# Optimization experiments

Hardware: AMD Instinct MI355X
Metric: run time of the kernel (lower is better)

## Reference

```python
import jax, jax.numpy as jnp
import numpy as np

N_NODES = 100000
N_EDGES = 600000
D_FEAT = 128
OUT_DIM = 128


def setup_inputs() -> dict:
    key = jax.random.key(0)
    k_x, k_r, k_c, k_v, k_w = jax.random.split(key, 5)
    x = jax.random.normal(k_x, (N_NODES, D_FEAT), dtype=jnp.float32)
    adj_rows = jax.random.randint(k_r, (N_EDGES,), 0, N_NODES, dtype=jnp.int64 if jax.config.jax_enable_x64 else jnp.int32).astype(jnp.int32)
    adj_cols = jax.random.randint(k_c, (N_EDGES,), 0, N_NODES, dtype=jnp.int32)
    adj_vals = jax.random.uniform(k_v, (N_EDGES,), dtype=jnp.float32)
    # Xavier-uniform init for W of shape [2*d, out]
    fan_in, fan_out = 2 * D_FEAT, OUT_DIM
    bound = float(np.sqrt(6.0 / (fan_in + fan_out)))
    W = jax.random.uniform(k_w, (2 * D_FEAT, OUT_DIM), minval=-bound, maxval=bound, dtype=jnp.float32)
    return {"x": x, "adj_rows": adj_rows, "adj_cols": adj_cols, "adj_vals": adj_vals, "W": W}


def reference(x, adj_rows, adj_cols, adj_vals, W):
    # h = A @ x  via COO SpMM: gather neighbor features, scale, segment-sum by row
    msgs = adj_vals[:, None] * x[adj_cols]            # [E, d]
    h = jax.ops.segment_sum(msgs, adj_rows, num_segments=N_NODES)  # [N, d]
    # concat([h, x]) @ W == h @ W[:d] + x @ W[d:]  (avoids materializing concat)
    out = h @ W[:D_FEAT] + x @ W[D_FEAT:]             # [N, out]
    return jax.nn.relu(out)
```

## Files before the change

### kernel.cpp

```cpp
#include <hip/hip_runtime.h>
#include <hip/hip_bf16.h>

constexpr int N_NODES = 100000;
constexpr int N_EDGES = 600000;
constexpr int D = 128;
constexpr int CAP = 32;

constexpr size_t X16_OFF  = 0;
constexpr size_t WP_OFF   = 25600000;
constexpr size_t CNT_OFF  = 25665536;
constexpr size_t BINS_OFF = 26065536;

typedef __attribute__((ext_vector_type(8))) short short8;
typedef __attribute__((ext_vector_type(4))) float float4v;

__device__ inline unsigned short f2bf(float f) {
    union { float f; unsigned int u; } v; v.f = f;
    unsigned int u = v.u + 0x7fffu + ((v.u >> 16) & 1u);
    return (unsigned short)(u >> 16);
}
__device__ inline float bf2f(unsigned int lo16) {
    union { unsigned int u; float f; } v; v.u = lo16 << 16;
    return v.f;
}

__global__ __launch_bounds__(256) void prep_kernel(
    const float* __restrict__ x, uint4* __restrict__ x16,
    const float* __restrict__ W, unsigned short* __restrict__ Wp,
    const int* __restrict__ rows, const int* __restrict__ cols,
    const float* __restrict__ vals,
    int* __restrict__ cnt, int2* __restrict__ bins)
{
    const int tid = blockIdx.x * 256 + threadIdx.x;
    const int T   = gridDim.x * 256;

    for (int e = tid; e < N_EDGES; e += T) {
        int r = rows[e];
        int pos = atomicAdd(&cnt[r], 1);
        if (pos < CAP)
            bins[(size_t)r * CAP + pos] = make_int2(cols[e], __float_as_int(vals[e]));
    }

    for (int idx = tid; idx < 8 * 8 * 64 * 8; idx += T) {
        int j    = idx & 7;
        int lane = (idx >> 3) & 63;
        int jt   = (idx >> 9) & 7;
        int s    = idx >> 12;
        int k = s * 32 + (lane >> 4) * 8 + j;
        int n = jt * 16 + (lane & 15);
        Wp[idx] = f2bf(W[k * 128 + n]);
    }

    for (int g = tid; g < N_NODES * D / 8; g += T) {
        const float4* xp = reinterpret_cast<const float4*>(x + (size_t)g * 8);
        float4 a = xp[0], c = xp[1];
        uint4 o;
        o.x = (unsigned int)f2bf(a.x) | ((unsigned int)f2bf(a.y) << 16);
        o.y = (unsigned int)f2bf(a.z) | ((unsigned int)f2bf(a.w) << 16);
        o.z = (unsigned int)f2bf(c.x) | ((unsigned int)f2bf(c.y) << 16);
        o.w = (unsigned int)f2bf(c.z) | ((unsigned int)f2bf(c.w) << 16);
        x16[g] = o;
    }
}

__global__ __launch_bounds__(128) void fused_agg_gemm_kernel(
    const uint4* __restrict__ x16v,
    const unsigned short* __restrict__ x16s,
    const int* __restrict__ cnt,
    const int2* __restrict__ bins,
    const unsigned short* __restrict__ Wp,
    float* __restrict__ out)
{
    __shared__ uint4 lds4[2 * 256];

    const int tid  = threadIdx.x;
    const int wave = tid >> 6;
    const int lane = tid & 63;
    const int row0 = blockIdx.x * 32 + wave * 16;

    {
        const int g   = lane >> 4;
        const int gl  = lane & 15;
        const int s_w = gl >> 2;
        const int q_w = gl & 3;

        int dends[4];
        const int4* b2[4];
        #pragma unroll
        for (int t = 0; t < 4; t++) {
            const int n = row0 + t * 4 + g;
            int d = cnt[n];
            dends[t] = d > CAP ? CAP : d;
            b2[t] = reinterpret_cast<const int4*>(bins + (size_t)n * CAP);
        }

        int4 nb0 = b2[0][0], nb1 = b2[0][1], nb2 = b2[0][2], nb3 = b2[0][3];

        #pragma unroll
        for (int t = 0; t < 4; t++) {
            const int m_local = t * 4 + g;
            const int dend = dends[t];

            const int4 c0 = nb0, c1 = nb1, c2 = nb2, c3 = nb3;
            if (t < 3) {
                nb0 = b2[t + 1][0]; nb1 = b2[t + 1][1];
                nb2 = b2[t + 1][2]; nb3 = b2[t + 1][3];
            }

            int col0 = c0.x; col0 = col0 < 0 ? 0 : col0;
            col0 = col0 >= N_NODES ? N_NODES - 1 : col0;
            const int cc1 = (1 < dend) ? c0.z : col0;
            const int cc2 = (2 < dend) ? c1.x : col0;
            const int cc3 = (3 < dend) ? c1.z : col0;
            const int cc4 = (4 < dend) ? c2.x : col0;
            const int cc5 = (5 < dend) ? c2.z : col0;
            const int cc6 = (6 < dend) ? c3.x : col0;
            const int cc7 = (7 < dend) ? c3.z : col0;
            const float v0 = (0 < dend) ? __int_as_float(c0.y) : 0.f;
            const float v1 = (1 < dend) ? __int_as_float(c0.w) : 0.f;
            const float v2 = (2 < dend) ? __int_as_float(c1.y) : 0.f;
            const float v3 = (3 < dend) ? __int_as_float(c1.w) : 0.f;
            const float v4 = (4 < dend) ? __int_as_float(c2.y) : 0.f;
            const float v5 = (5 < dend) ? __int_as_float(c2.w) : 0.f;
            const float v6 = (6 < dend) ? __int_as_float(c3.y) : 0.f;
            const float v7 = (7 < dend) ? __int_as_float(c3.w) : 0.f;

            const uint4 p0 = x16v[(size_t)col0 * 16 + gl];
            const uint4 p1 = x16v[(size_t)cc1  * 16 + gl];
            const uint4 p2 = x16v[(size_t)cc2  * 16 + gl];
            const uint4 p3 = x16v[(size_t)cc3  * 16 + gl];
            const uint4 p4 = x16v[(size_t)cc4  * 16 + gl];
            const uint4 p5 = x16v[(size_t)cc5  * 16 + gl];
            const uint4 p6 = x16v[(size_t)cc6  * 16 + gl];
            const uint4 p7 = x16v[(size_t)cc7  * 16 + gl];

            float a0, a1, a2, a3, a4, a5, a6, a7;
            a0  = v0 * bf2f(p0.x & 0xffffu) + v1 * bf2f(p1.x & 0xffffu)
                + v2 * bf2f(p2.x & 0xffffu) + v3 * bf2f(p3.x & 0xffffu)
                + v4 * bf2f(p4.x & 0xffffu) + v5 * bf2f(p5.x & 0xffffu)
                + v6 * bf2f(p6.x & 0xffffu) + v7 * bf2f(p7.x & 0xffffu);
            a1  = v0 * bf2f(p0.x >> 16)     + v1 * bf2f(p1.x >> 16)
                + v2 * bf2f(p2.x >> 16)     + v3 * bf2f(p3.x >> 16)
                + v4 * bf2f(p4.x >> 16)     + v5 * bf2f(p5.x >> 16)
                + v6 * bf2f(p6.x >> 16)     + v7 * bf2f(p7.x >> 16);
            a2  = v0 * bf2f(p0.y & 0xffffu) + v1 * bf2f(p1.y & 0xffffu)
                + v2 * bf2f(p2.y & 0xffffu) + v3 * bf2f(p3.y & 0xffffu)
                + v4 * bf2f(p4.y & 0xffffu) + v5 * bf2f(p5.y & 0xffffu)
                + v6 * bf2f(p6.y & 0xffffu) + v7 * bf2f(p7.y & 0xffffu);
            a3  = v0 * bf2f(p0.y >> 16)     + v1 * bf2f(p1.y >> 16)
                + v2 * bf2f(p2.y >> 16)     + v3 * bf2f(p3.y >> 16)
                + v4 * bf2f(p4.y >> 16)     + v5 * bf2f(p5.y >> 16)
                + v6 * bf2f(p6.y >> 16)     + v7 * bf2f(p7.y >> 16);
            a4  = v0 * bf2f(p0.z & 0xffffu) + v1 * bf2f(p1.z & 0xffffu)
                + v2 * bf2f(p2.z & 0xffffu) + v3 * bf2f(p3.z & 0xffffu)
                + v4 * bf2f(p4.z & 0xffffu) + v5 * bf2f(p5.z & 0xffffu)
                + v6 * bf2f(p6.z & 0xffffu) + v7 * bf2f(p7.z & 0xffffu);
            a5  = v0 * bf2f(p0.z >> 16)     + v1 * bf2f(p1.z >> 16)
                + v2 * bf2f(p2.z >> 16)     + v3 * bf2f(p3.z >> 16)
                + v4 * bf2f(p4.z >> 16)     + v5 * bf2f(p5.z >> 16)
                + v6 * bf2f(p6.z >> 16)     + v7 * bf2f(p7.z >> 16);
            a6  = v0 * bf2f(p0.w & 0xffffu) + v1 * bf2f(p1.w & 0xffffu)
                + v2 * bf2f(p2.w & 0xffffu) + v3 * bf2f(p3.w & 0xffffu)
                + v4 * bf2f(p4.w & 0xffffu) + v5 * bf2f(p5.w & 0xffffu)
                + v6 * bf2f(p6.w & 0xffffu) + v7 * bf2f(p7.w & 0xffffu);
            a7  = v0 * bf2f(p0.w >> 16)     + v1 * bf2f(p1.w >> 16)
                + v2 * bf2f(p2.w >> 16)     + v3 * bf2f(p3.w >> 16)
                + v4 * bf2f(p4.w >> 16)     + v5 * bf2f(p5.w >> 16)
                + v6 * bf2f(p6.w >> 16)     + v7 * bf2f(p7.w >> 16);

            if (dend > 8) {
                const int2* bp = bins + (size_t)(row0 + m_local) * CAP;
                for (int i = 8; i < dend; i += 4) {
                    const int i1 = (i + 1 < dend) ? i + 1 : dend - 1;
                    const int i2 = (i + 2 < dend) ? i + 2 : dend - 1;
                    const int i3 = (i + 3 < dend) ? i + 3 : dend - 1;
                    int2 e0 = bp[i];
                    int2 e1 = bp[i1];
                    int2 e2 = bp[i2];
                    int2 e3 = bp[i3];
                    uint4 q0 = x16v[(size_t)e0.x * 16 + gl];
                    uint4 q1 = x16v[(size_t)e1.x * 16 + gl];
                    uint4 q2 = x16v[(size_t)e2.x * 16 + gl];
                    uint4 q3 = x16v[(size_t)e3.x * 16 + gl];
                    float w0 = __int_as_float(e0.y);
                    float w1 = (i + 1 < dend) ? __int_as_float(e1.y) : 0.f;
                    float w2 = (i + 2 < dend) ? __int_as_float(e2.y) : 0.f;
                    float w3 = (i + 3 < dend) ? __int_as_float(e3.y) : 0.f;
                    a0 += w0 * bf2f(q0.x & 0xffffu) + w1 * bf2f(q1.x & 0xffffu)
                        + w2 * bf2f(q2.x & 0xffffu) + w3 * bf2f(q3.x & 0xffffu);
                    a1 += w0 * bf2f(q0.x >> 16)     + w1 * bf2f(q1.x >> 16)
                        + w2 * bf2f(q2.x >> 16)     + w3 * bf2f(q3.x >> 16);
                    a2 += w0 * bf2f(q0.y & 0xffffu) + w1 * bf2f(q1.y & 0xffffu)
                        + w2 * bf2f(q2.y & 0xffffu) + w3 * bf2f(q3.y & 0xffffu);
                    a3 += w0 * bf2f(q0.y >> 16)     + w1 * bf2f(q1.y >> 16)
                        + w2 * bf2f(q2.y >> 16)     + w3 * bf2f(q3.y >> 16);
                    a4 += w0 * bf2f(q0.z & 0xffffu) + w1 * bf2f(q1.z & 0xffffu)
                        + w2 * bf2f(q2.z & 0xffffu) + w3 * bf2f(q3.z & 0xffffu);
                    a5 += w0 * bf2f(q0.z >> 16)     + w1 * bf2f(q1.z >> 16)
                        + w2 * bf2f(q2.z >> 16)     + w3 * bf2f(q3.z >> 16);
                    a6 += w0 * bf2f(q0.w & 0xffffu) + w1 * bf2f(q1.w & 0xffffu)
                        + w2 * bf2f(q2.w & 0xffffu) + w3 * bf2f(q3.w & 0xffffu);
                    a7 += w0 * bf2f(q0.w >> 16)     + w1 * bf2f(q1.w >> 16)
                        + w2 * bf2f(q2.w >> 16)     + w3 * bf2f(q3.w >> 16);
                }
            }

            uint4 o;
            o.x = (unsigned int)f2bf(a0) | ((unsigned int)f2bf(a1) << 16);
            o.y = (unsigned int)f2bf(a2) | ((unsigned int)f2bf(a3) << 16);
            o.z = (unsigned int)f2bf(a4) | ((unsigned int)f2bf(a5) << 16);
            o.w = (unsigned int)f2bf(a6) | ((unsigned int)f2bf(a7) << 16);
            lds4[wave * 256 + s_w * 64 + m_local * 4 + q_w] = o;
        }
    }
    __syncthreads();

    const int m    = lane & 15;
    const int quad = lane >> 4;

    const unsigned short* xrow = x16s + (size_t)(row0 + m) * D + quad * 8;

    float4v acc[8];
    #pragma unroll
    for (int jt = 0; jt < 8; jt++) acc[jt] = (float4v){0.f, 0.f, 0.f, 0.f};

    #pragma unroll
    for (int s = 0; s < 8; s++) {
        short8 a;
        if (s < 4)
            a = *reinterpret_cast<const short8*>(&lds4[wave * 256 + s * 64 + m * 4 + quad]);
        else
            a = *reinterpret_cast<const short8*>(xrow + (s - 4) * 32);
        #pragma unroll
        for (int jt = 0; jt < 8; jt++) {
            short8 b = *reinterpret_cast<const short8*>(
                Wp + ((size_t)((s * 8 + jt) * 64 + lane)) * 8);
            acc[jt] = __builtin_amdgcn_mfma_f32_16x16x32_bf16(a, b, acc[jt], 0, 0, 0);
        }
    }

    #pragma unroll
    for (int reg = 0; reg < 4; reg++) {
        const int r = row0 + quad * 4 + reg;
        float* orow = out + (size_t)r * D;
        #pragma unroll
        for (int jt = 0; jt < 8; jt++)
            orow[jt * 16 + m] = fmaxf(acc[jt][reg], 0.f);
    }
}

extern "C" void kernel_launch(void* const* d_in, const int* in_sizes, int n_in,
                              void* d_out, int out_size, void* d_ws, size_t ws_size,
                              hipStream_t stream)
{
    const float* x    = (const float*)d_in[0];
    const int*   rows = (const int*)  d_in[1];
    const int*   cols = (const int*)  d_in[2];
    const float* vals = (const float*)d_in[3];
    const float* W    = (const float*)d_in[4];
    float* out = (float*)d_out;

    char* ws = (char*)d_ws;
    uint4*          x16v = (uint4*)         (ws + X16_OFF);
    unsigned short* x16s = (unsigned short*)(ws + X16_OFF);
    unsigned short* Wp   = (unsigned short*)(ws + WP_OFF);
    int*            cnt  = (int*)           (ws + CNT_OFF);
    int2*           bins = (int2*)          (ws + BINS_OFF);

    hipMemsetAsync(cnt, 0, N_NODES * sizeof(int), stream);
    prep_kernel<<<2048, 256, 0, stream>>>(x, x16v, W, Wp, rows, cols, vals, cnt, bins);
    fused_agg_gemm_kernel<<<N_NODES / 32, 128, 0, stream>>>(
        x16v, x16s, cnt, bins, Wp, out);
}
```

Measured before the change: 185.2 us.

## Partition edge binning by row range and split GEMM columns across waves

```diff
diff --git a/kernel.cpp b/kernel.cpp
--- a/kernel.cpp
+++ b/kernel.cpp
@@ -5,6 +5,8 @@
 constexpr int N_EDGES = 600000;
 constexpr int D = 128;
 constexpr int CAP = 32;
+constexpr int NRANGE = 8;
+constexpr int ROWS_PER_RANGE = N_NODES / NRANGE;
 
 constexpr size_t X16_OFF  = 0;
 constexpr size_t WP_OFF   = 25600000;
@@ -34,13 +36,6 @@
     const int tid = blockIdx.x * 256 + threadIdx.x;
     const int T   = gridDim.x * 256;
 
-    for (int e = tid; e < N_EDGES; e += T) {
-        int r = rows[e];
-        int pos = atomicAdd(&cnt[r], 1);
-        if (pos < CAP)
-            bins[(size_t)r * CAP + pos] = make_int2(cols[e], __float_as_int(vals[e]));
-    }
-
     for (int idx = tid; idx < 8 * 8 * 64 * 8; idx += T) {
         int j    = idx & 7;
         int lane = (idx >> 3) & 63;
@@ -61,9 +56,29 @@
         o.w = (unsigned int)f2bf(c.z) | ((unsigned int)f2bf(c.w) << 16);
         x16[g] = o;
     }
-}
-
-__global__ __launch_bounds__(128) void fused_agg_gemm_kernel(
+
+    {
+        const int p   = blockIdx.x & 7;
+        const int rlo = p * ROWS_PER_RANGE;
+        const int rhi = rlo + ROWS_PER_RANGE;
+        const int sb  = (int)(blockIdx.x >> 3);
+        const int nsl = (int)(gridDim.x >> 3);
+        const int elen = (N_EDGES + nsl - 1) / nsl;
+        const int e0 = sb * elen;
+        int e1 = e0 + elen; if (e1 > N_EDGES) e1 = N_EDGES;
+        for (int e = e0 + threadIdx.x; e < e1; e += 256) {
+            int r = rows[e];
+            if (r >= rlo && r < rhi) {
+                int pos = atomicAdd(&cnt[r], 1);
+                if (pos < CAP)
+                    bins[(size_t)r * CAP + pos] =
+                        make_int2(cols[e], __float_as_int(vals[e]));
+            }
+        }
+    }
+}
+
+__global__ __launch_bounds__(256) void fused_agg_gemm_kernel(
     const uint4* __restrict__ x16v,
     const unsigned short* __restrict__ x16s,
     const int* __restrict__ cnt,
@@ -71,181 +86,161 @@
     const unsigned short* __restrict__ Wp,
     float* __restrict__ out)
 {
-    __shared__ uint4 lds4[2 * 256];
+    __shared__ uint4 lds4[256];
 
     const int tid  = threadIdx.x;
     const int wave = tid >> 6;
     const int lane = tid & 63;
-    const int row0 = blockIdx.x * 32 + wave * 16;
+    const int row0 = blockIdx.x * 16;
 
     {
-        const int g   = lane >> 4;
-        const int gl  = lane & 15;
-        const int s_w = gl >> 2;
-        const int q_w = gl & 3;
-
-        int dends[4];
-        const int4* b2[4];
-        #pragma unroll
-        for (int t = 0; t < 4; t++) {
-            const int n = row0 + t * 4 + g;
-            int d = cnt[n];
-            dends[t] = d > CAP ? CAP : d;
-            b2[t] = reinterpret_cast<const int4*>(bins + (size_t)n * CAP);
+        const int G  = wave * 4 + (lane >> 4);
+        const int gl = lane & 15;
+        const int n  = row0 + G;
+
+        const int4* b2 = reinterpret_cast<const int4*>(bins + (size_t)n * CAP);
+        const int  d   = cnt[n];
+        const int4 c0 = b2[0], c1 = b2[1], c2 = b2[2], c3 = b2[3];
+        const int dend = d > CAP ? CAP : d;
+
+        int col0 = c0.x; col0 = col0 < 0 ? 0 : col0;
+        col0 = col0 >= N_NODES ? N_NODES - 1 : col0;
+        const int cc1 = (1 < dend) ? c0.z : col0;
+        const int cc2 = (2 < dend) ? c1.x : col0;
+        const int cc3 = (3 < dend) ? c1.z : col0;
+        const int cc4 = (4 < dend) ? c2.x : col0;
+        const int cc5 = (5 < dend) ? c2.z : col0;
+        const int cc6 = (6 < dend) ? c3.x : col0;
+        const int cc7 = (7 < dend) ? c3.z : col0;
+        const float v0 = (0 < dend) ? __int_as_float(c0.y) : 0.f;
+        const float v1 = (1 < dend) ? __int_as_float(c0.w) : 0.f;
+        const float v2 = (2 < dend) ? __int_as_float(c1.y) : 0.f;
+        const float v3 = (3 < dend) ? __int_as_float(c1.w) : 0.f;
+        const float v4 = (4 < dend) ? __int_as_float(c2.y) : 0.f;
+        const float v5 = (5 < dend) ? __int_as_float(c2.w) : 0.f;
+        const float v6 = (6 < dend) ? __int_as_float(c3.y) : 0.f;
+        const float v7 = (7 < dend) ? __int_as_float(c3.w) : 0.f;
+
+        const uint4 p0 = x16v[(size_t)col0 * 16 + gl];
+        const uint4 p1 = x16v[(size_t)cc1  * 16 + gl];
+        const uint4 p2 = x16v[(size_t)cc2  * 16 + gl];
+        const uint4 p3 = x16v[(size_t)cc3  * 16 + gl];
+        const uint4 p4 = x16v[(size_t)cc4  * 16 + gl];
+        const uint4 p5 = x16v[(size_t)cc5  * 16 + gl];
+        const uint4 p6 = x16v[(size_t)cc6  * 16 + gl];
+        const uint4 p7 = x16v[(size_t)cc7  * 16 + gl];
+
+        float a0, a1, a2, a3, a4, a5, a6, a7;
+        a0  = v0 * bf2f(p0.x & 0xffffu) + v1 * bf2f(p1.x & 0xffffu)
+            + v2 * bf2f(p2.x & 0xffffu) + v3 * bf2f(p3.x & 0xffffu)
+            + v4 * bf2f(p4.x & 0xffffu) + v5 * bf2f(p5.x & 0xffffu)
+            + v6 * bf2f(p6.x & 0xffffu) + v7 * bf2f(p7.x & 0xffffu);
+        a1  = v0 * bf2f(p0.x >> 16)     + v1 * bf2f(p1.x >> 16)
+            + v2 * bf2f(p2.x >> 16)     + v3 * bf2f(p3.x >> 16)
+            + v4 * bf2f(p4.x >> 16)     + v5 * bf2f(p5.x >> 16)
+            + v6 * bf2f(p6.x >> 16)     + v7 * bf2f(p7.x >> 16);
+        a2  = v0 * bf2f(p0.y & 0xffffu) + v1 * bf2f(p1.y & 0xffffu)
+            + v2 * bf2f(p2.y & 0xffffu) + v3 * bf2f(p3.y & 0xffffu)
+            + v4 * bf2f(p4.y & 0xffffu) + v5 * bf2f(p5.y & 0xffffu)
+            + v6 * bf2f(p6.y & 0xffffu) + v7 * bf2f(p7.y & 0xffffu);
+        a3  = v0 * bf2f(p0.y >> 16)     + v1 * bf2f(p1.y >> 16)
+            + v2 * bf2f(p2.y >> 16)     + v3 * bf2f(p3.y >> 16)
+            + v4 * bf2f(p4.y >> 16)     + v5 * bf2f(p5.y >> 16)
+            + v6 * bf2f(p6.y >> 16)     + v7 * bf2f(p7.y >> 16);
+        a4  = v0 * bf2f(p0.z & 0xffffu) + v1 * bf2f(p1.z & 0xffffu)
+            + v2 * bf2f(p2.z & 0xffffu) + v3 * bf2f(p3.z & 0xffffu)
+            + v4 * bf2f(p4.z & 0xffffu) + v5 * bf2f(p5.z & 0xffffu)
+            + v6 * bf2f(p6.z & 0xffffu) + v7 * bf2f(p7.z & 0xffffu);
+        a5  = v0 * bf2f(p0.z >> 16)     + v1 * bf2f(p1.z >> 16)
+            + v2 * bf2f(p2.z >> 16)     + v3 * bf2f(p3.z >> 16)
+            + v4 * bf2f(p4.z >> 16)     + v5 * bf2f(p5.z >> 16)
+            + v6 * bf2f(p6.z >> 16)     + v7 * bf2f(p7.z >> 16);
+        a6  = v0 * bf2f(p0.w & 0xffffu) + v1 * bf2f(p1.w & 0xffffu)
+            + v2 * bf2f(p2.w & 0xffffu) + v3 * bf2f(p3.w & 0xffffu)
+            + v4 * bf2f(p4.w & 0xffffu) + v5 * bf2f(p5.w & 0xffffu)
+            + v6 * bf2f(p6.w & 0xffffu) + v7 * bf2f(p7.w & 0xffffu);
+        a7  = v0 * bf2f(p0.w >> 16)     + v1 * bf2f(p1.w >> 16)
+            + v2 * bf2f(p2.w >> 16)     + v3 * bf2f(p3.w >> 16)
+            + v4 * bf2f(p4.w >> 16)     + v5 * bf2f(p5.w >> 16)
+            + v6 * bf2f(p6.w >> 16)     + v7 * bf2f(p7.w >> 16);
+
+        if (dend > 8) {
+            const int2* bp = bins + (size_t)n * CAP;
+            for (int i = 8; i < dend; i += 4) {
+                const int i1 = (i + 1 < dend) ? i + 1 : dend - 1;
+                const int i2 = (i + 2 < dend) ? i + 2 : dend - 1;
+                const int i3 = (i + 3 < dend) ? i + 3 : dend - 1;
+                int2 e0 = bp[i];
+                int2 e1 = bp[i1];
+                int2 e2 = bp[i2];
+                int2 e3 = bp[i3];
+                uint4 q0 = x16v[(size_t)e0.x * 16 + gl];
+                uint4 q1 = x16v[(size_t)e1.x * 16 + gl];
+                uint4 q2 = x16v[(size_t)e2.x * 16 + gl];
+                uint4 q3 = x16v[(size_t)e3.x * 16 + gl];
+                float w0 = __int_as_float(e0.y);
+                float w1 = (i + 1 < dend) ? __int_as_float(e1.y) : 0.f;
+                float w2 = (i + 2 < dend) ? __int_as_float(e2.y) : 0.f;
+                float w3 = (i + 3 < dend) ? __int_as_float(e3.y) : 0.f;
+                a0 += w0 * bf2f(q0.x & 0xffffu) + w1 * bf2f(q1.x & 0xffffu)
+                    + w2 * bf2f(q2.x & 0xffffu) + w3 * bf2f(q3.x & 0xffffu);
+                a1 += w0 * bf2f(q0.x >> 16)     + w1 * bf2f(q1.x >> 16)
+                    + w2 * bf2f(q2.x >> 16)     + w3 * bf2f(q3.x >> 16);
+                a2 += w0 * bf2f(q0.y & 0xffffu) + w1 * bf2f(q1.y & 0xffffu)
+                    + w2 * bf2f(q2.y & 0xffffu) + w3 * bf2f(q3.y & 0xffffu);
+                a3 += w0 * bf2f(q0.y >> 16)     + w1 * bf2f(q1.y >> 16)
+                    + w2 * bf2f(q2.y >> 16)     + w3 * bf2f(q3.y >> 16);
+                a4 += w0 * bf2f(q0.z & 0xffffu) + w1 * bf2f(q1.z & 0xffffu)
+                    + w2 * bf2f(q2.z & 0xffffu) + w3 * bf2f(q3.z & 0xffffu);
+                a5 += w0 * bf2f(q0.z >> 16)     + w1 * bf2f(q1.z >> 16)
+                    + w2 * bf2f(q2.z >> 16)     + w3 * bf2f(q3.z >> 16);
+                a6 += w0 * bf2f(q0.w & 0xffffu) + w1 * bf2f(q1.w & 0xffffu)
+                    + w2 * bf2f(q2.w & 0xffffu) + w3 * bf2f(q3.w & 0xffffu);
+                a7 += w0 * bf2f(q0.w >> 16)     + w1 * bf2f(q1.w >> 16)
+                    + w2 * bf2f(q2.w >> 16)     + w3 * bf2f(q3.w >> 16);
+            }
         }
 
-        int4 nb0 = b2[0][0], nb1 = b2[0][1], nb2 = b2[0][2], nb3 = b2[0][3];
-
-        #pragma unroll
-        for (int t = 0; t < 4; t++) {
-            const int m_local = t * 4 + g;
-            const int dend = dends[t];
-
-            const int4 c0 = nb0, c1 = nb1, c2 = nb2, c3 = nb3;
-            if (t < 3) {
-                nb0 = b2[t + 1][0]; nb1 = b2[t + 1][1];
-                nb2 = b2[t + 1][2]; nb3 = b2[t + 1][3];
-            }
-
-            int col0 = c0.x; col0 = col0 < 0 ? 0 : col0;
-            col0 = col0 >= N_NODES ? N_NODES - 1 : col0;
-            const int cc1 = (1 < dend) ? c0.z : col0;
-            const int cc2 = (2 < dend) ? c1.x : col0;
-            const int cc3 = (3 < dend) ? c1.z : col0;
-            const int cc4 = (4 < dend) ? c2.x : col0;
-            const int cc5 = (5 < dend) ? c2.z : col0;
-            const int cc6 = (6 < dend) ? c3.x : col0;
-            const int cc7 = (7 < dend) ? c3.z : col0;
-            const float v0 = (0 < dend) ? __int_as_float(c0.y) : 0.f;
-            const float v1 = (1 < dend) ? __int_as_float(c0.w) : 0.f;
-            const float v2 = (2 < dend) ? __int_as_float(c1.y) : 0.f;
-            const float v3 = (3 < dend) ? __int_as_float(c1.w) : 0.f;
-            const float v4 = (4 < dend) ? __int_as_float(c2.y) : 0.f;
-            const float v5 = (5 < dend) ? __int_as_float(c2.w) : 0.f;
-            const float v6 = (6 < dend) ? __int_as_float(c3.y) : 0.f;
-            const float v7 = (7 < dend) ? __int_as_float(c3.w) : 0.f;
-
-            const uint4 p0 = x16v[(size_t)col0 * 16 + gl];
-            const uint4 p1 = x16v[(size_t)cc1  * 16 + gl];
-            const uint4 p2 = x16v[(size_t)cc2  * 16 + gl];
-            const uint4 p3 = x16v[(size_t)cc3  * 16 + gl];
-            const uint4 p4 = x16v[(size_t)cc4  * 16 + gl];
-            const uint4 p5 = x16v[(size_t)cc5  * 16 + gl];
-            const uint4 p6 = x16v[(size_t)cc6  * 16 + gl];
-            const uint4 p7 = x16v[(size_t)cc7  * 16 + gl];
-
-            float a0, a1, a2, a3, a4, a5, a6, a7;
-            a0  = v0 * bf2f(p0.x & 0xffffu) + v1 * bf2f(p1.x & 0xffffu)
-                + v2 * bf2f(p2.x & 0xffffu) + v3 * bf2f(p3.x & 0xffffu)
-                + v4 * bf2f(p4.x & 0xffffu) + v5 * bf2f(p5.x & 0xffffu)
-                + v6 * bf2f(p6.x & 0xffffu) + v7 * bf2f(p7.x & 0xffffu);
-            a1  = v0 * bf2f(p0.x >> 16)     + v1 * bf2f(p1.x >> 16)
-                + v2 * bf2f(p2.x >> 16)     + v3 * bf2f(p3.x >> 16)
-                + v4 * bf2f(p4.x >> 16)     + v5 * bf2f(p5.x >> 16)
-                + v6 * bf2f(p6.x >> 16)     + v7 * bf2f(p7.x >> 16);
-            a2  = v0 * bf2f(p0.y & 0xffffu) + v1 * bf2f(p1.y & 0xffffu)
-                + v2 * bf2f(p2.y & 0xffffu) + v3 * bf2f(p3.y & 0xffffu)
-                + v4 * bf2f(p4.y & 0xffffu) + v5 * bf2f(p5.y & 0xffffu)
-                + v6 * bf2f(p6.y & 0xffffu) + v7 * bf2f(p7.y & 0xffffu);
-            a3  = v0 * bf2f(p0.y >> 16)     + v1 * bf2f(p1.y >> 16)
-                + v2 * bf2f(p2.y >> 16)     + v3 * bf2f(p3.y >> 16)
-                + v4 * bf2f(p4.y >> 16)     + v5 * bf2f(p5.y >> 16)
-                + v6 * bf2f(p6.y >> 16)     + v7 * bf2f(p7.y >> 16);
-            a4  = v0 * bf2f(p0.z & 0xffffu) + v1 * bf2f(p1.z & 0xffffu)
-                + v2 * bf2f(p2.z & 0xffffu) + v3 * bf2f(p3.z & 0xffffu)
-                + v4 * bf2f(p4.z & 0xffffu) + v5 * bf2f(p5.z & 0xffffu)
-                + v6 * bf2f(p6.z & 0xffffu) + v7 * bf2f(p7.z & 0xffffu);
-            a5  = v0 * bf2f(p0.z >> 16)     + v1 * bf2f(p1.z >> 16)
-                + v2 * bf2f(p2.z >> 16)     + v3 * bf2f(p3.z >> 16)
-                + v4 * bf2f(p4.z >> 16)     + v5 * bf2f(p5.z >> 16)
-                + v6 * bf2f(p6.z >> 16)     + v7 * bf2f(p7.z >> 16);
-            a6  = v0 * bf2f(p0.w & 0xffffu) + v1 * bf2f(p1.w & 0xffffu)
-                + v2 * bf2f(p2.w & 0xffffu) + v3 * bf2f(p3.w & 0xffffu)
-                + v4 * bf2f(p4.w & 0xffffu) + v5 * bf2f(p5.w & 0xffffu)
-                + v6 * bf2f(p6.w & 0xffffu) + v7 * bf2f(p7.w & 0xffffu);
-            a7  = v0 * bf2f(p0.w >> 16)     + v1 * bf2f(p1.w >> 16)
-                + v2 * bf2f(p2.w >> 16)     + v3 * bf2f(p3.w >> 16)
-                + v4 * bf2f(p4.w >> 16)     + v5 * bf2f(p5.w >> 16)
-                + v6 * bf2f(p6.w >> 16)     + v7 * bf2f(p7.w >> 16);
-
-            if (dend > 8) {
-                const int2* bp = bins + (size_t)(row0 + m_local) * CAP;
-                for (int i = 8; i < dend; i += 4) {
-                    const int i1 = (i + 1 < dend) ? i + 1 : dend - 1;
-                    const int i2 = (i + 2 < dend) ? i + 2 : dend - 1;
-                    const int i3 = (i + 3 < dend) ? i + 3 : dend - 1;
-                    int2 e0 = bp[i];
-                    int2 e1 = bp[i1];
-                    int2 e2 = bp[i2];
-                    int2 e3 = bp[i3];
-                    uint4 q0 = x16v[(size_t)e0.x * 16 + gl];
-                    uint4 q1 = x16v[(size_t)e1.x * 16 + gl];
-                    uint4 q2 = x16v[(size_t)e2.x * 16 + gl];
-                    uint4 q3 = x16v[(size_t)e3.x * 16 + gl];
-                    float w0 = __int_as_float(e0.y);
-                    float w1 = (i + 1 < dend) ? __int_as_float(e1.y) : 0.f;
-                    float w2 = (i + 2 < dend) ? __int_as_float(e2.y) : 0.f;
-                    float w3 = (i + 3 < dend) ? __int_as_float(e3.y) : 0.f;
-                    a0 += w0 * bf2f(q0.x & 0xffffu) + w1 * bf2f(q1.x & 0xffffu)
-                        + w2 * bf2f(q2.x & 0xffffu) + w3 * bf2f(q3.x & 0xffffu);
-                    a1 += w0 * bf2f(q0.x >> 16)     + w1 * bf2f(q1.x >> 16)
-                        + w2 * bf2f(q2.x >> 16)     + w3 * bf2f(q3.x >> 16);
-                    a2 += w0 * bf2f(q0.y & 0xffffu) + w1 * bf2f(q1.y & 0xffffu)
-                        + w2 * bf2f(q2.y & 0xffffu) + w3 * bf2f(q3.y & 0xffffu);
-                    a3 += w0 * bf2f(q0.y >> 16)     + w1 * bf2f(q1.y >> 16)
-                        + w2 * bf2f(q2.y >> 16)     + w3 * bf2f(q3.y >> 16);
-                    a4 += w0 * bf2f(q0.z & 0xffffu) + w1 * bf2f(q1.z & 0xffffu)
-                        + w2 * bf2f(q2.z & 0xffffu) + w3 * bf2f(q3.z & 0xffffu);
-                    a5 += w0 * bf2f(q0.z >> 16)     + w1 * bf2f(q1.z >> 16)
-                        + w2 * bf2f(q2.z >> 16)     + w3 * bf2f(q3.z >> 16);
-                    a6 += w0 * bf2f(q0.w & 0xffffu) + w1 * bf2f(q1.w & 0xffffu)
-                        + w2 * bf2f(q2.w & 0xffffu) + w3 * bf2f(q3.w & 0xffffu);
-                    a7 += w0 * bf2f(q0.w >> 16)     + w1 * bf2f(q1.w >> 16)
-                        + w2 * bf2f(q2.w >> 16)     + w3 * bf2f(q3.w >> 16);
-                }
-            }
-
-            uint4 o;
-            o.x = (unsigned int)f2bf(a0) | ((unsigned int)f2bf(a1) << 16);
-            o.y = (unsigned int)f2bf(a2) | ((unsigned int)f2bf(a3) << 16);
-            o.z = (unsigned int)f2bf(a4) | ((unsigned int)f2bf(a5) << 16);
-            o.w = (unsigned int)f2bf(a6) | ((unsigned int)f2bf(a7) << 16);
-            lds4[wave * 256 + s_w * 64 + m_local * 4 + q_w] = o;
-        }
+        uint4 o;
+        o.x = (unsigned int)f2bf(a0) | ((unsigned int)f2bf(a1) << 16);
+        o.y = (unsigned int)f2bf(a2) | ((unsigned int)f2bf(a3) << 16);
+        o.z = (unsigned int)f2bf(a4) | ((unsigned int)f2bf(a5) << 16);
+        o.w = (unsigned int)f2bf(a6) | ((unsigned int)f2bf(a7) << 16);
+        lds4[(gl >> 2) * 64 + G * 4 + (gl & 3)] = o;
     }
     __syncthreads();
 
     const int m    = lane & 15;
     const int quad = lane >> 4;
+    const int jt0  = wave * 2;
+    const int jt1  = jt0 + 1;
 
     const unsigned short* xrow = x16s + (size_t)(row0 + m) * D + quad * 8;
 
-    float4v acc[8];
-    #pragma unroll
-    for (int jt = 0; jt < 8; jt++) acc[jt] = (float4v){0.f, 0.f, 0.f, 0.f};
+    float4v acc0 = (float4v){0.f, 0.f, 0.f, 0.f};
+    float4v acc1 = (float4v){0.f, 0.f, 0.f, 0.f};
 
     #pragma unroll
     for (int s = 0; s < 8; s++) {
         short8 a;
         if (s < 4)
-            a = *reinterpret_cast<const short8*>(&lds4[wave * 256 + s * 64 + m * 4 + quad]);
+            a = *reinterpret_cast<const short8*>(&lds4[s * 64 + m * 4 + quad]);
         else
             a = *reinterpret_cast<const short8*>(xrow + (s - 4) * 32);
-        #pragma unroll
-        for (int jt = 0; jt < 8; jt++) {
-            short8 b = *reinterpret_cast<const short8*>(
-                Wp + ((size_t)((s * 8 + jt) * 64 + lane)) * 8);
-            acc[jt] = __builtin_amdgcn_mfma_f32_16x16x32_bf16(a, b, acc[jt], 0, 0, 0);
-        }
+        short8 b0 = *reinterpret_cast<const short8*>(
+            Wp + ((size_t)((s * 8 + jt0) * 64 + lane)) * 8);
+        short8 b1 = *reinterpret_cast<const short8*>(
+            Wp + ((size_t)((s * 8 + jt1) * 64 + lane)) * 8);
+        acc0 = __builtin_amdgcn_mfma_f32_16x16x32_bf16(a, b0, acc0, 0, 0, 0);
+        acc1 = __builtin_amdgcn_mfma_f32_16x16x32_bf16(a, b1, acc1, 0, 0, 0);
     }
 
     #pragma unroll
     for (int reg = 0; reg < 4; reg++) {
         const int r = row0 + quad * 4 + reg;
         float* orow = out + (size_t)r * D;
-        #pragma unroll
-        for (int jt = 0; jt < 8; jt++)
-            orow[jt * 16 + m] = fmaxf(acc[jt][reg], 0.f);
+        orow[jt0 * 16 + m] = fmaxf(acc0[reg], 0.f);
+        orow[jt1 * 16 + m] = fmaxf(acc1[reg], 0.f);
     }
 }
 
@@ -269,6 +264,6 @@
 
     hipMemsetAsync(cnt, 0, N_NODES * sizeof(int), stream);
     prep_kernel<<<2048, 256, 0, stream>>>(x, x16v, W, Wp, rows, cols, vals, cnt, bins);
-    fused_agg_gemm_kernel<<<N_NODES / 32, 128, 0, stream>>>(
+    fused_agg_gemm_kernel<<<N_NODES / 16, 256, 0, stream>>>(
         x16v, x16s, cnt, bins, Wp, out);
 }
```

New measurement: 189.4 us. 1.02x slower.
